# Performance work log

Measured on AMD Instinct MI355X. Metric: run time of the kernel, lower is better.

## Reference

```python
import jax, jax.numpy as jnp
import numpy as np

B, S, D, H = 8, 1024, 1024, 16
HD = D // H  # head dim = 64


def setup_inputs() -> dict:
    key = jax.random.key(0)
    ks = jax.random.split(key, 8)
    return {
        "hidden_states": jax.random.normal(ks[0], (B, S, D), dtype=jnp.float32),
        "attention_mask": jnp.zeros((B, 1, 1, S), dtype=jnp.float32),
        "Wq": jax.random.normal(ks[1], (D, D), dtype=jnp.float32) * (1.0 / np.sqrt(D)),
        "bq": jax.random.normal(ks[2], (D,), dtype=jnp.float32) * 0.02,
        "Wk": jax.random.normal(ks[3], (D, D), dtype=jnp.float32) * (1.0 / np.sqrt(D)),
        "bk": jax.random.normal(ks[4], (D,), dtype=jnp.float32) * 0.02,
        "Wv": jax.random.normal(ks[5], (D, D), dtype=jnp.float32) * (1.0 / np.sqrt(D)),
        "bv": jax.random.normal(ks[6], (D,), dtype=jnp.float32) * 0.02,
    }


def _split_heads(x):
    # [B,S,D] -> [B,H,S,HD]
    return x.reshape(B, S, H, HD).transpose(0, 2, 1, 3)


def reference(hidden_states, attention_mask, Wq, bq, Wk, bk, Wv, bv):
    q = _split_heads(hidden_states @ Wq + bq)
    k = _split_heads(hidden_states @ Wk + bk)
    v = _split_heads(hidden_states @ Wv + bv)
    # [B,H,S,S]
    scores = jnp.einsum("bhqd,bhkd->bhqk", q, k) / jnp.sqrt(jnp.float32(HD))
    scores = scores + attention_mask
    probs = jax.nn.softmax(scores, axis=-1)  # dropout p=0.0 (eval)
    ctx = jnp.einsum("bhqk,bhkd->bhqd", probs, v)
    # [B,H,S,HD] -> [B,S,D]
    return ctx.transpose(0, 2, 1, 3).reshape(B, S, D)
```

## Files before the change

### kernel.cpp

```cpp
#include <hip/hip_runtime.h>
#include <stdint.h>

#define BB 8
#define SS 1024
#define DD 1024
#define HH 16
#define HDIM 64

typedef __bf16 bf16x8 __attribute__((ext_vector_type(8)));
typedef float f32x4 __attribute__((ext_vector_type(4)));

__device__ __forceinline__ unsigned short f2bf(float f) {
    union { float f; unsigned u; } v; v.f = f;
    unsigned r = v.u + 0x7fff + ((v.u >> 16) & 1);
    return (unsigned short)(r >> 16);
}

__device__ __forceinline__ void async16(void* lds, const void* g) {
    __builtin_amdgcn_global_load_lds(
        (const __attribute__((address_space(1))) unsigned int*)g,
        (__attribute__((address_space(3))) unsigned int*)lds, 16, 0, 0);
}

__global__ __launch_bounds__(256) void convert_x(const float* __restrict__ x,
                                                 unsigned short* __restrict__ xb, int n) {
    int i = (blockIdx.x * 256 + threadIdx.x) * 4;
    if (i < n) {
        float4 f = *reinterpret_cast<const float4*>(x + i);
        ushort4 o;
        o.x = f2bf(f.x); o.y = f2bf(f.y); o.z = f2bf(f.z); o.w = f2bf(f.w);
        *reinterpret_cast<ushort4*>(xb + i) = o;
    }
}

__global__ __launch_bounds__(256) void transpose_w(const float* __restrict__ w0,
                                                   const float* __restrict__ w1,
                                                   const float* __restrict__ w2,
                                                   unsigned short* __restrict__ t0,
                                                   unsigned short* __restrict__ t1,
                                                   unsigned short* __restrict__ t2) {
    const float* w = (blockIdx.z == 0) ? w0 : (blockIdx.z == 1) ? w1 : w2;
    unsigned short* wt = (blockIdx.z == 0) ? t0 : (blockIdx.z == 1) ? t1 : t2;
    __shared__ unsigned short tile[64][65];
    int k0 = blockIdx.x * 64, n0 = blockIdx.y * 64;
    #pragma unroll
    for (int i = 0; i < 16; ++i) {
        int idx = threadIdx.x + i * 256;
        int r = idx >> 6, c = idx & 63;
        tile[r][c] = f2bf(w[(k0 + r) * DD + n0 + c]);
    }
    __syncthreads();
    #pragma unroll
    for (int i = 0; i < 16; ++i) {
        int idx = threadIdx.x + i * 256;
        int r = idx >> 6, c = idx & 63;
        wt[(n0 + r) * DD + k0 + c] = tile[c][r];
    }
}

__global__ __launch_bounds__(256) void gemm_qkv(
    const unsigned short* __restrict__ xb,
    const unsigned short* __restrict__ wt0, const unsigned short* __restrict__ wt1,
    const unsigned short* __restrict__ wt2,
    const float* __restrict__ b0, const float* __restrict__ b1, const float* __restrict__ b2,
    unsigned short* __restrict__ qo, unsigned short* __restrict__ ko,
    unsigned short* __restrict__ vto)
{
    const unsigned short* wt; const float* bias; unsigned short* out;
    if (blockIdx.z == 0)      { wt = wt0; bias = b0; out = qo; }
    else if (blockIdx.z == 1) { wt = wt1; bias = b1; out = ko; }
    else                      { wt = wt2; bias = b2; out = vto; }

    __shared__ unsigned short As[128 * 32];
    __shared__ unsigned short Bs[128 * 32];

    int m0 = blockIdx.x * 128, n0 = blockIdx.y * 128;
    int tid = threadIdx.x;
    int wave = tid >> 6, lane = tid & 63, lq = lane >> 4, lm = lane & 15;
    int wr = wave >> 1, wc = wave & 1;

    f32x4 acc[4][4] = {};

    int id0 = tid, id1 = tid + 256;
    const unsigned short* ga0 = xb + (m0 + (id0 >> 2)) * DD + (id0 & 3) * 8;
    const unsigned short* ga1 = xb + (m0 + (id1 >> 2)) * DD + (id1 & 3) * 8;
    const unsigned short* gb0 = wt + (n0 + (id0 >> 2)) * DD + (id0 & 3) * 8;
    const unsigned short* gb1 = wt + (n0 + (id1 >> 2)) * DD + (id1 & 3) * 8;

    for (int k0 = 0; k0 < DD; k0 += 32) {
        async16(&As[id0 * 8], ga0 + k0);
        async16(&As[id1 * 8], ga1 + k0);
        async16(&Bs[id0 * 8], gb0 + k0);
        async16(&Bs[id1 * 8], gb1 + k0);
        __syncthreads();
        bf16x8 a[4], b[4];
        #pragma unroll
        for (int i = 0; i < 4; ++i)
            a[i] = *reinterpret_cast<const bf16x8*>(&As[(wr * 64 + i * 16 + lm) * 32 + lq * 8]);
        #pragma unroll
        for (int j = 0; j < 4; ++j)
            b[j] = *reinterpret_cast<const bf16x8*>(&Bs[(wc * 64 + j * 16 + lm) * 32 + lq * 8]);
        #pragma unroll
        for (int i = 0; i < 4; ++i)
            #pragma unroll
            for (int j = 0; j < 4; ++j)
                acc[i][j] = __builtin_amdgcn_mfma_f32_16x16x32_bf16(a[i], b[j], acc[i][j], 0, 0, 0);
        __syncthreads();
    }

    if (blockIdx.z == 2) {
        #pragma unroll
        for (int j = 0; j < 4; ++j) {
            int col = n0 + wc * 64 + j * 16 + lm;
            float bsv = bias[col];
            int h = col >> 6, hd = col & 63;
            #pragma unroll
            for (int i = 0; i < 4; ++i) {
                int m = m0 + wr * 64 + i * 16 + lq * 4;
                int b_ = m >> 10, sr = m & 1023;
                ushort4 pk;
                pk.x = f2bf(acc[i][j][0] + bsv);
                pk.y = f2bf(acc[i][j][1] + bsv);
                pk.z = f2bf(acc[i][j][2] + bsv);
                pk.w = f2bf(acc[i][j][3] + bsv);
                *reinterpret_cast<ushort4*>(out + (((b_ * HH + h) * HDIM + hd) << 10) + sr) = pk;
            }
        }
    } else {
        #pragma unroll
        for (int j = 0; j < 4; ++j) {
            int col = n0 + wc * 64 + j * 16 + lm;
            float bsv = bias[col];
            int h = col >> 6, hd = col & 63;
            #pragma unroll
            for (int i = 0; i < 4; ++i) {
                #pragma unroll
                for (int r = 0; r < 4; ++r) {
                    int m = m0 + wr * 64 + i * 16 + lq * 4 + r;
                    int b_ = m >> 10, sr = m & 1023;
                    out[(((b_ * HH + h) << 10) + sr) * HDIM + hd] = f2bf(acc[i][j][r] + bsv);
                }
            }
        }
    }
}

__global__ __launch_bounds__(256) void attention(
    const unsigned short* __restrict__ q,
    const unsigned short* __restrict__ k,
    const unsigned short* __restrict__ vt,
    const float* __restrict__ mask,
    float* __restrict__ out)
{
    __shared__ unsigned short Ks[64 * 80];
    __shared__ unsigned short Vs[64 * 72];
    __shared__ unsigned short Ps[4 * 16 * 72];
    __shared__ float msk[SS];

    int bh = blockIdx.y;
    int b = bh >> 4, h = bh & 15;
    int qt = blockIdx.x;
    int tid = threadIdx.x;
    int wave = tid >> 6, lane = tid & 63, lq = lane >> 4, lm = lane & 15;

    const unsigned short* qp = q + (size_t)bh * SS * HDIM;
    const unsigned short* kp = k + (size_t)bh * SS * HDIM;
    const unsigned short* vp = vt + (size_t)bh * HDIM * SS;

    for (int i = tid; i < SS; i += 256) msk[i] = mask[b * SS + i];

    int qrow = qt * 64 + wave * 16 + lm;
    bf16x8 qa0 = *reinterpret_cast<const bf16x8*>(qp + qrow * HDIM + lq * 8);
    bf16x8 qa1 = *reinterpret_cast<const bf16x8*>(qp + qrow * HDIM + 32 + lq * 8);

    float lsum[4] = {0.f, 0.f, 0.f, 0.f};
    f32x4 o[4] = {};

    int id0 = tid, id1 = tid + 256;
    int k0r = id0 >> 3, k0c = (id0 & 7) * 8;
    int k1r = id1 >> 3, k1c = (id1 & 7) * 8;
    unsigned short* Pw = &Ps[wave * 16 * 72];

    for (int kb0 = 0; kb0 < SS; kb0 += 64) {
        *reinterpret_cast<uint4*>(&Ks[k0r * 80 + k0c]) =
            *reinterpret_cast<const uint4*>(kp + (kb0 + k0r) * HDIM + k0c);
        *reinterpret_cast<uint4*>(&Ks[k1r * 80 + k1c]) =
            *reinterpret_cast<const uint4*>(kp + (kb0 + k1r) * HDIM + k1c);
        *reinterpret_cast<uint4*>(&Vs[k0r * 72 + k0c]) =
            *reinterpret_cast<const uint4*>(vp + k0r * SS + kb0 + k0c);
        *reinterpret_cast<uint4*>(&Vs[k1r * 72 + k1c]) =
            *reinterpret_cast<const uint4*>(vp + k1r * SS + kb0 + k1c);
        __syncthreads();

        f32x4 c[4] = {};
        #pragma unroll
        for (int nb = 0; nb < 4; ++nb) {
            bf16x8 kf0 = *reinterpret_cast<const bf16x8*>(&Ks[(nb * 16 + lm) * 80 + lq * 8]);
            bf16x8 kf1 = *reinterpret_cast<const bf16x8*>(&Ks[(nb * 16 + lm) * 80 + 32 + lq * 8]);
            c[nb] = __builtin_amdgcn_mfma_f32_16x16x32_bf16(qa0, kf0, c[nb], 0, 0, 0);
            c[nb] = __builtin_amdgcn_mfma_f32_16x16x32_bf16(qa1, kf1, c[nb], 0, 0, 0);
        }

        #pragma unroll
        for (int nb = 0; nb < 4; ++nb) {
            float mk = msk[kb0 + nb * 16 + lm];
            #pragma unroll
            for (int r = 0; r < 4; ++r) {
                float p = __expf(c[nb][r] * 0.125f + mk);
                lsum[r] += p;
                Pw[(lq * 4 + r) * 72 + nb * 16 + lm] = f2bf(p);
            }
        }
        #pragma unroll
        for (int ks = 0; ks < 2; ++ks) {
            bf16x8 pa = *reinterpret_cast<const bf16x8*>(&Pw[lm * 72 + ks * 32 + lq * 8]);
            #pragma unroll
            for (int nb2 = 0; nb2 < 4; ++nb2) {
                bf16x8 vf = *reinterpret_cast<const bf16x8*>(&Vs[(nb2 * 16 + lm) * 72 + ks * 32 + lq * 8]);
                o[nb2] = __builtin_amdgcn_mfma_f32_16x16x32_bf16(pa, vf, o[nb2], 0, 0, 0);
            }
        }
        __syncthreads();
    }

    #pragma unroll
    for (int r = 0; r < 4; ++r) {
        float s = lsum[r];
        #pragma unroll
        for (int d = 1; d < 16; d <<= 1) s += __shfl_xor(s, d, 64);
        lsum[r] = s;
    }

    #pragma unroll
    for (int nb2 = 0; nb2 < 4; ++nb2) {
        #pragma unroll
        for (int r = 0; r < 4; ++r) {
            int sr = qt * 64 + wave * 16 + lq * 4 + r;
            out[((size_t)(b * SS + sr)) * DD + h * HDIM + nb2 * 16 + lm] = o[nb2][r] / lsum[r];
        }
    }
}

extern "C" void kernel_launch(void* const* d_in, const int* in_sizes, int n_in,
                              void* d_out, int out_size, void* d_ws, size_t ws_size,
                              hipStream_t stream) {
    const float* hs   = (const float*)d_in[0];
    const float* mask = (const float*)d_in[1];
    const float* Wq   = (const float*)d_in[2];
    const float* bq   = (const float*)d_in[3];
    const float* Wk   = (const float*)d_in[4];
    const float* bk   = (const float*)d_in[5];
    const float* Wv   = (const float*)d_in[6];
    const float* bv   = (const float*)d_in[7];
    float* out = (float*)d_out;

    char* ws = (char*)d_ws;
    unsigned short* Xb  = (unsigned short*)(ws);
    unsigned short* WT0 = (unsigned short*)(ws + 16777216);
    unsigned short* WT1 = (unsigned short*)(ws + 18874368);
    unsigned short* WT2 = (unsigned short*)(ws + 20971520);
    unsigned short* qw  = (unsigned short*)(ws + 23068672);
    unsigned short* kw  = (unsigned short*)(ws + 39845888);
    unsigned short* vtw = (unsigned short*)(ws + 56623104);

    convert_x<<<8192, 256, 0, stream>>>(hs, Xb, BB * SS * DD);
    transpose_w<<<dim3(16, 16, 3), 256, 0, stream>>>(Wq, Wk, Wv, WT0, WT1, WT2);
    gemm_qkv<<<dim3(64, 8, 3), 256, 0, stream>>>(Xb, WT0, WT1, WT2,
                                                 bq, bk, bv, qw, kw, vtw);
    attention<<<dim3(16, 128), 256, 0, stream>>>(qw, kw, vtw, mask, out);
}
```

Measured before the change: 258.7 us.

## Double-buffer GEMM and attention tiles, swizzle LDS, remap blocks per XCD, use exp2

```diff
diff --git a/kernel.cpp b/kernel.cpp
--- a/kernel.cpp
+++ b/kernel.cpp
@@ -14,6 +14,14 @@
     union { float f; unsigned u; } v; v.f = f;
     unsigned r = v.u + 0x7fff + ((v.u >> 16) & 1);
     return (unsigned short)(r >> 16);
+}
+
+__device__ __forceinline__ float exp2fast(float x) {
+#if __has_builtin(__builtin_amdgcn_exp2f)
+    return __builtin_amdgcn_exp2f(x);
+#else
+    return __expf(x * 0.69314718f);
+#endif
 }
 
 __device__ __forceinline__ void async16(void* lds, const void* g) {
@@ -71,8 +79,8 @@
     else if (blockIdx.z == 1) { wt = wt1; bias = b1; out = ko; }
     else                      { wt = wt2; bias = b2; out = vto; }
 
-    __shared__ unsigned short As[128 * 32];
-    __shared__ unsigned short Bs[128 * 32];
+    __shared__ unsigned short As[2][128 * 32];
+    __shared__ unsigned short Bs[2][128 * 32];
 
     int m0 = blockIdx.x * 128, n0 = blockIdx.y * 128;
     int tid = threadIdx.x;
@@ -81,31 +89,39 @@
 
     f32x4 acc[4][4] = {};
 
-    int id0 = tid, id1 = tid + 256;
-    const unsigned short* ga0 = xb + (m0 + (id0 >> 2)) * DD + (id0 & 3) * 8;
-    const unsigned short* ga1 = xb + (m0 + (id1 >> 2)) * DD + (id1 & 3) * 8;
-    const unsigned short* gb0 = wt + (n0 + (id0 >> 2)) * DD + (id0 & 3) * 8;
-    const unsigned short* gb1 = wt + (n0 + (id1 >> 2)) * DD + (id1 & 3) * 8;
-
-    for (int k0 = 0; k0 < DD; k0 += 32) {
-        async16(&As[id0 * 8], ga0 + k0);
-        async16(&As[id1 * 8], ga1 + k0);
-        async16(&Bs[id0 * 8], gb0 + k0);
-        async16(&Bs[id1 * 8], gb1 + k0);
+    int row0 = tid >> 2, s = tid & 3;
+    int c0 = (s - (row0 >> 1)) & 3;
+    const unsigned short* ga0 = xb + (m0 + row0) * DD + c0 * 8;
+    const unsigned short* ga1 = ga0 + 64 * DD;
+    const unsigned short* gb0 = wt + (n0 + row0) * DD + c0 * 8;
+    const unsigned short* gb1 = gb0 + 64 * DD;
+
+    int slot = ((lq + (lm >> 1)) & 3) * 8;
+
+    async16(&As[0][tid * 8], ga0);  async16(&As[0][(tid + 256) * 8], ga1);
+    async16(&Bs[0][tid * 8], gb0);  async16(&Bs[0][(tid + 256) * 8], gb1);
+    ga0 += 32; ga1 += 32; gb0 += 32; gb1 += 32;
+
+    for (int t = 0; t < 32; ++t) {
+        int p = t & 1;
         __syncthreads();
+        if (t < 31) {
+            async16(&As[p ^ 1][tid * 8], ga0);  async16(&As[p ^ 1][(tid + 256) * 8], ga1);
+            async16(&Bs[p ^ 1][tid * 8], gb0);  async16(&Bs[p ^ 1][(tid + 256) * 8], gb1);
+            ga0 += 32; ga1 += 32; gb0 += 32; gb1 += 32;
+        }
         bf16x8 a[4], b[4];
         #pragma unroll
         for (int i = 0; i < 4; ++i)
-            a[i] = *reinterpret_cast<const bf16x8*>(&As[(wr * 64 + i * 16 + lm) * 32 + lq * 8]);
+            a[i] = *reinterpret_cast<const bf16x8*>(&As[p][(wr * 64 + i * 16 + lm) * 32 + slot]);
         #pragma unroll
         for (int j = 0; j < 4; ++j)
-            b[j] = *reinterpret_cast<const bf16x8*>(&Bs[(wc * 64 + j * 16 + lm) * 32 + lq * 8]);
+            b[j] = *reinterpret_cast<const bf16x8*>(&Bs[p][(wc * 64 + j * 16 + lm) * 32 + slot]);
         #pragma unroll
         for (int i = 0; i < 4; ++i)
             #pragma unroll
             for (int j = 0; j < 4; ++j)
                 acc[i][j] = __builtin_amdgcn_mfma_f32_16x16x32_bf16(a[i], b[j], acc[i][j], 0, 0, 0);
-        __syncthreads();
     }
 
     if (blockIdx.z == 2) {
@@ -152,14 +168,17 @@
     const float* __restrict__ mask,
     float* __restrict__ out)
 {
-    __shared__ unsigned short Ks[64 * 80];
-    __shared__ unsigned short Vs[64 * 72];
-    __shared__ unsigned short Ps[4 * 16 * 72];
+    __shared__ unsigned short Ks[2][64 * 64];
+    __shared__ unsigned short Vs[2][64 * 64];
+    __shared__ unsigned short Ps[4][16 * 72];
     __shared__ float msk[SS];
 
-    int bh = blockIdx.y;
+    int blk = blockIdx.x;
+    int xcd = blk & 7, j = blk >> 3;
+    int bh = (xcd << 4) + (j >> 4);
+    int qt = j & 15;
     int b = bh >> 4, h = bh & 15;
-    int qt = blockIdx.x;
+
     int tid = threadIdx.x;
     int wave = tid >> 6, lane = tid & 63, lq = lane >> 4, lm = lane & 15;
 
@@ -167,76 +186,94 @@
     const unsigned short* kp = k + (size_t)bh * SS * HDIM;
     const unsigned short* vp = vt + (size_t)bh * HDIM * SS;
 
-    for (int i = tid; i < SS; i += 256) msk[i] = mask[b * SS + i];
+    for (int i = tid; i < SS; i += 256) msk[i] = mask[b * SS + i] * 1.44269504f;
 
     int qrow = qt * 64 + wave * 16 + lm;
     bf16x8 qa0 = *reinterpret_cast<const bf16x8*>(qp + qrow * HDIM + lq * 8);
     bf16x8 qa1 = *reinterpret_cast<const bf16x8*>(qp + qrow * HDIM + 32 + lq * 8);
 
-    float lsum[4] = {0.f, 0.f, 0.f, 0.f};
+    float lsum = 0.f;
     f32x4 o[4] = {};
 
-    int id0 = tid, id1 = tid + 256;
-    int k0r = id0 >> 3, k0c = (id0 & 7) * 8;
-    int k1r = id1 >> 3, k1c = (id1 & 7) * 8;
-    unsigned short* Pw = &Ps[wave * 16 * 72];
-
-    for (int kb0 = 0; kb0 < SS; kb0 += 64) {
-        *reinterpret_cast<uint4*>(&Ks[k0r * 80 + k0c]) =
-            *reinterpret_cast<const uint4*>(kp + (kb0 + k0r) * HDIM + k0c);
-        *reinterpret_cast<uint4*>(&Ks[k1r * 80 + k1c]) =
-            *reinterpret_cast<const uint4*>(kp + (kb0 + k1r) * HDIM + k1c);
-        *reinterpret_cast<uint4*>(&Vs[k0r * 72 + k0c]) =
-            *reinterpret_cast<const uint4*>(vp + k0r * SS + kb0 + k0c);
-        *reinterpret_cast<uint4*>(&Vs[k1r * 72 + k1c]) =
-            *reinterpret_cast<const uint4*>(vp + k1r * SS + kb0 + k1c);
+    int row0 = tid >> 3, sg = tid & 7;
+    int cg = (sg - row0) & 7;
+    const unsigned short* gk = kp + row0 * 64 + cg * 8;
+    const unsigned short* gv = vp + row0 * SS + cg * 8;
+
+    int sl0 = ((lq + lm) & 7) * 8;
+    int sl1 = ((lq + lm + 4) & 7) * 8;
+
+    async16(&Ks[0][tid * 8], gk);  async16(&Ks[0][(tid + 256) * 8], gk + 32 * 64);
+    async16(&Vs[0][tid * 8], gv);  async16(&Vs[0][(tid + 256) * 8], gv + 32 * SS);
+    gk += 64 * 64; gv += 64;
+
+    unsigned short* Pw = Ps[wave];
+
+    for (int t = 0; t < 16; ++t) {
+        int p = t & 1;
         __syncthreads();
-
-        f32x4 c[4] = {};
+        if (t < 15) {
+            async16(&Ks[p ^ 1][tid * 8], gk);  async16(&Ks[p ^ 1][(tid + 256) * 8], gk + 32 * 64);
+            async16(&Vs[p ^ 1][tid * 8], gv);  async16(&Vs[p ^ 1][(tid + 256) * 8], gv + 32 * SS);
+            gk += 64 * 64; gv += 64;
+        }
+        int kb0 = t * 64;
+
+        f32x4 c[4];
         #pragma unroll
         for (int nb = 0; nb < 4; ++nb) {
-            bf16x8 kf0 = *reinterpret_cast<const bf16x8*>(&Ks[(nb * 16 + lm) * 80 + lq * 8]);
-            bf16x8 kf1 = *reinterpret_cast<const bf16x8*>(&Ks[(nb * 16 + lm) * 80 + 32 + lq * 8]);
-            c[nb] = __builtin_amdgcn_mfma_f32_16x16x32_bf16(qa0, kf0, c[nb], 0, 0, 0);
-            c[nb] = __builtin_amdgcn_mfma_f32_16x16x32_bf16(qa1, kf1, c[nb], 0, 0, 0);
+            bf16x8 kf0 = *reinterpret_cast<const bf16x8*>(&Ks[p][(nb * 16 + lm) * 64 + sl0]);
+            bf16x8 kf1 = *reinterpret_cast<const bf16x8*>(&Ks[p][(nb * 16 + lm) * 64 + sl1]);
+            f32x4 z = {};
+            z = __builtin_amdgcn_mfma_f32_16x16x32_bf16(kf0, qa0, z, 0, 0, 0);
+            z = __builtin_amdgcn_mfma_f32_16x16x32_bf16(kf1, qa1, z, 0, 0, 0);
+            c[nb] = z;
         }
 
         #pragma unroll
         for (int nb = 0; nb < 4; ++nb) {
-            float mk = msk[kb0 + nb * 16 + lm];
+            float4 mk = *reinterpret_cast<const float4*>(&msk[kb0 + nb * 16 + lq * 4]);
+            unsigned u[4];
             #pragma unroll
             for (int r = 0; r < 4; ++r) {
-                float p = __expf(c[nb][r] * 0.125f + mk);
-                lsum[r] += p;
-                Pw[(lq * 4 + r) * 72 + nb * 16 + lm] = f2bf(p);
+                float e = exp2fast(fmaf(c[nb][r], 0.18033688f,
+                                        reinterpret_cast<const float*>(&mk)[r]));
+                union { float f; unsigned v; } cv; cv.f = e;
+                u[r] = cv.v;
+                union { unsigned v; float f; } tr; tr.v = cv.v & 0xffff0000u;
+                lsum += tr.f;
             }
-        }
+            uint2 pk;
+            pk.x = __builtin_amdgcn_perm(u[1], u[0], 0x07060302u);
+            pk.y = __builtin_amdgcn_perm(u[3], u[2], 0x07060302u);
+            *reinterpret_cast<uint2*>(&Pw[lm * 72 + nb * 16 + lq * 4]) = pk;
+        }
+
         #pragma unroll
         for (int ks = 0; ks < 2; ++ks) {
             bf16x8 pa = *reinterpret_cast<const bf16x8*>(&Pw[lm * 72 + ks * 32 + lq * 8]);
+            int slv = (ks == 0) ? sl0 : sl1;
             #pragma unroll
             for (int nb2 = 0; nb2 < 4; ++nb2) {
-                bf16x8 vf = *reinterpret_cast<const bf16x8*>(&Vs[(nb2 * 16 + lm) * 72 + ks * 32 + lq * 8]);
+                bf16x8 vf = *reinterpret_cast<const bf16x8*>(&Vs[p][(nb2 * 16 + lm) * 64 + slv]);
                 o[nb2] = __builtin_amdgcn_mfma_f32_16x16x32_bf16(pa, vf, o[nb2], 0, 0, 0);
             }
         }
-        __syncthreads();
-    }
-
+    }
+
+    lsum += __shfl_xor(lsum, 16, 64);
+    lsum += __shfl_xor(lsum, 32, 64);
+    float linv[4];
     #pragma unroll
-    for (int r = 0; r < 4; ++r) {
-        float s = lsum[r];
-        #pragma unroll
-        for (int d = 1; d < 16; d <<= 1) s += __shfl_xor(s, d, 64);
-        lsum[r] = s;
-    }
+    for (int r = 0; r < 4; ++r)
+        linv[r] = 1.0f / __shfl(lsum, lq * 4 + r, 64);
 
     #pragma unroll
     for (int nb2 = 0; nb2 < 4; ++nb2) {
         #pragma unroll
         for (int r = 0; r < 4; ++r) {
             int sr = qt * 64 + wave * 16 + lq * 4 + r;
-            out[((size_t)(b * SS + sr)) * DD + h * HDIM + nb2 * 16 + lm] = o[nb2][r] / lsum[r];
+            out[((size_t)(b * SS + sr)) * DD + h * HDIM + nb2 * 16 + lm] = o[nb2][r] * linv[r];
         }
     }
 }
@@ -267,5 +304,5 @@
     transpose_w<<<dim3(16, 16, 3), 256, 0, stream>>>(Wq, Wk, Wv, WT0, WT1, WT2);
     gemm_qkv<<<dim3(64, 8, 3), 256, 0, stream>>>(Xb, WT0, WT1, WT2,
                                                  bq, bk, bv, qw, kw, vtw);
-    attention<<<dim3(16, 128), 256, 0, stream>>>(qw, kw, vtw, mask, out);
-}
+    attention<<<2048, 256, 0, stream>>>(qw, kw, vtw, mask, out);
+}
```

Result: faster. 249.3 us (-3.6%).
